# Optimization experiments

Measured on AMD Instinct MI355X. Metric: run time of the kernel, lower is better.

## Reference

```python
import jax, jax.numpy as jnp
from jax import lax
import numpy as np

RANK = 128
INPUT_DIM = 128
OUT_DIM = 32
N = 128
L = 512
INIT_STD = 1.0 / np.sqrt(RANK * INPUT_DIM)  # variance-preserving recurrence


def setup_inputs() -> dict:
    key = jax.random.key(0)
    k_x, k_A, k_a, k_O = jax.random.split(key, 4)
    x = jax.random.normal(k_x, (N, L, INPUT_DIM), dtype=jnp.float32)
    A = INIT_STD * jax.random.normal(k_A, (RANK, INPUT_DIM, RANK), dtype=jnp.float32)
    alpha = INIT_STD * jax.random.normal(k_a, (RANK,), dtype=jnp.float32)
    Omega = INIT_STD * jax.random.normal(k_O, (RANK, OUT_DIM), dtype=jnp.float32)
    return {"x": x, "alpha": alpha, "A": A, "Omega": Omega}


def reference(x, alpha, A, Omega):
    # x: [N, L, D]; alpha: [R]; A: [R, D, R]; Omega: [R, M]
    # h_0 = einsum('i,ijk,nj->nk', alpha, A, x[:,0])
    h0 = jnp.einsum('i,ijk,nj->nk', alpha, A, x[:, 0, :])

    def step(h, xt):
        # h: [N, R], xt: [N, D] -> new h: [N, R]
        h = jnp.einsum('ni,ijk,nj->nk', h, A, xt)
        return h, None

    xs = jnp.swapaxes(x, 0, 1)[1:]  # [L-1, N, D]
    h, _ = lax.scan(step, h0, xs)
    out = jnp.einsum('ni,im->nm', h, Omega)  # [N, M]
    return jnp.squeeze(out)
```

## Files before the change

kernel.cpp:

```cpp
#include <hip/hip_runtime.h>

typedef _Float16 f16;
typedef _Float16 half8 __attribute__((ext_vector_type(8)));
typedef _Float16 half4v __attribute__((ext_vector_type(4)));
typedef float f32x4 __attribute__((ext_vector_type(4)));


__global__ void k_cvt_x(const float* __restrict__ in, f16* __restrict__ out) {
    int idx = blockIdx.x * blockDim.x + threadIdx.x;
    float4 v = ((const float4*)in)[idx];
    half4v o;
    o[0] = (f16)v.x; o[1] = (f16)v.y; o[2] = (f16)v.z; o[3] = (f16)v.w;
    ((half4v*)out)[idx] = o;
}

__global__ void k_cvt_A(const float* __restrict__ A, f16* __restrict__ Af2) {
    int o = blockIdx.x * blockDim.x + threadIdx.x;
    int i = o >> 14;
    int k = (o >> 7) & 127;
    int j = o & 127;
    Af2[o] = (f16)A[(i << 14) + (j << 7) + k];
}

__device__ __forceinline__
void gemm_body(f16* lA, f16* lX, const f16* __restrict__ Af2, const f16* __restrict__ Xh,
               f16* __restrict__ B, int t0, int logTc, int qtile, int i, int tid) {
    const int row = tid >> 4;
    const int ch = tid & 15;
    const int Tcm1 = (1 << logTc) - 1;

    {
        const f16* srcA = Af2 + ((size_t)i << 14);
#pragma unroll
        for (int r = 0; r < 128; r += 16) {
            int rr = row + r;
            uint4 v = *(const uint4*)(srcA + (rr << 7) + (ch << 3));
            *(uint4*)(&lA[(rr << 7) + ((ch ^ (rr & 15)) << 3)]) = v;
        }
#pragma unroll
        for (int r = 0; r < 128; r += 16) {
            int rr = row + r;
            int qr = (qtile << 7) + rr;
            int n = qr >> logTc;
            int trel = qr & Tcm1;
            const f16* srcX = Xh + (((size_t)(n << 9) + t0 + trel) << 7);
            uint4 v = *(const uint4*)(srcX + (ch << 3));
            *(uint4*)(&lX[(rr << 7) + ((ch ^ (rr & 15)) << 3)]) = v;
        }
    }
    __syncthreads();

    const int wave = tid >> 6;
    const int lane = tid & 63;
    const int l15 = lane & 15;
    const int l4 = lane >> 4;
    f32x4 acc[8][2] = {};

#pragma unroll
    for (int ks = 0; ks < 4; ++ks) {
        const int c = (ks << 2) + l4;
        half8 afr[8], bfr[2];
#pragma unroll
        for (int mt = 0; mt < 8; ++mt) {
            int rowA = (mt << 4) + l15;
            afr[mt] = *(const half8*)(&lA[(rowA << 7) + ((c ^ l15) << 3)]);
        }
#pragma unroll
        for (int qt = 0; qt < 2; ++qt) {
            int rowX = (wave << 5) + (qt << 4) + l15;
            bfr[qt] = *(const half8*)(&lX[(rowX << 7) + ((c ^ l15) << 3)]);
        }
#pragma unroll
        for (int mt = 0; mt < 8; ++mt)
#pragma unroll
            for (int qt = 0; qt < 2; ++qt)
                acc[mt][qt] = __builtin_amdgcn_mfma_f32_16x16x32_f16(
                    afr[mt], bfr[qt], acc[mt][qt], 0, 0, 0);
    }

    __syncthreads();
    f16* stage = lA;
#pragma unroll
    for (int mt = 0; mt < 8; ++mt)
#pragma unroll
        for (int qt = 0; qt < 2; ++qt) {
            int q = (wave << 5) + (qt << 4) + l15;
            int chunk = (mt << 1) + (l4 >> 1);
            int hf = l4 & 1;
            half4v o;
            o[0] = (f16)acc[mt][qt][0];
            o[1] = (f16)acc[mt][qt][1];
            o[2] = (f16)acc[mt][qt][2];
            o[3] = (f16)acc[mt][qt][3];
            *(half4v*)(&stage[(q << 7) + (((chunk ^ l15) << 3) + (hf << 2))]) = o;
        }
    __syncthreads();
    {
        const int lr = lane >> 4;
        const int lc = lane & 15;
#pragma unroll
        for (int it = 0; it < 8; ++it) {
            int q = (wave << 5) + (it << 2) + lr;
            uint4 v = *(const uint4*)(&stage[(q << 7) + ((lc ^ (q & 15)) << 3)]);
            size_t qg = (size_t)((qtile << 7) + q);
            *(uint4*)(B + (qg << 14) + (i << 7) + (lc << 3)) = v;
        }
    }
}

__device__ __forceinline__
void chain_body(float* hl, float (*part)[132], const f16* __restrict__ B,
                float* __restrict__ hstate, const float* __restrict__ alpha,
                const float* __restrict__ Om, float* __restrict__ out,
                int Tc, int first, int last, int n, int tid) {
    const int kg = tid & 15;
    const int iq = tid >> 4;

    if (tid < 128) hl[tid] = first ? alpha[tid] : hstate[(n << 7) + tid];
    __syncthreads();

    const f16* bbase = B + (((size_t)n * Tc) << 14) + (iq << 10) + (kg << 3);
    half8 buf[4][8];
#pragma unroll
    for (int s = 0; s < 4; ++s)
#pragma unroll
        for (int ii = 0; ii < 8; ++ii)
            buf[s][ii] = *(const half8*)(bbase + ((size_t)s << 14) + (ii << 7));

    for (int t = 0; t < Tc; t += 4) {
#pragma unroll
        for (int s = 0; s < 4; ++s) {
            float4 h0 = *(const float4*)&hl[iq << 3];
            float4 h1 = *(const float4*)&hl[(iq << 3) + 4];
            float acc[8] = {0, 0, 0, 0, 0, 0, 0, 0};
#pragma unroll
            for (int ii = 0; ii < 4; ++ii) {
                float hv = (&h0.x)[ii];
#pragma unroll
                for (int j = 0; j < 8; ++j)
                    acc[j] += hv * (float)buf[s][ii][j];
            }
#pragma unroll
            for (int ii = 0; ii < 4; ++ii) {
                float hv = (&h1.x)[ii];
#pragma unroll
                for (int j = 0; j < 8; ++j)
                    acc[j] += hv * (float)buf[s][ii + 4][j];
            }
            int tn = t + s + 4;
            if (tn < Tc) {
#pragma unroll
                for (int ii = 0; ii < 8; ++ii)
                    buf[s][ii] = *(const half8*)(bbase + ((size_t)tn << 14) + (ii << 7));
            }
            *(float4*)(&part[iq][kg << 3])       = make_float4(acc[0], acc[1], acc[2], acc[3]);
            *(float4*)(&part[iq][(kg << 3) + 4]) = make_float4(acc[4], acc[5], acc[6], acc[7]);
            __syncthreads();
            if (tid < 128) {
                float s0 = part[0][tid] + part[1][tid];
                float s1 = part[2][tid] + part[3][tid];
                float s2 = part[4][tid] + part[5][tid];
                float s3 = part[6][tid] + part[7][tid];
                s0 += part[8][tid] + part[9][tid];
                s1 += part[10][tid] + part[11][tid];
                s2 += part[12][tid] + part[13][tid];
                s3 += part[14][tid] + part[15][tid];
                hl[tid] = (s0 + s1) + (s2 + s3);
            }
            __syncthreads();
        }
    }

    if (!last) {
        if (tid < 128) hstate[(n << 7) + tid] = hl[tid];
    } else if (tid < 32) {
        float s = 0.f;
        for (int i2 = 0; i2 < 128; ++i2) s += hl[i2] * Om[(i2 << 5) + tid];
        out[(n << 5) + tid] = s;
    }
}

__global__ __launch_bounds__(256, 2)
void k_gemm(const f16* __restrict__ Af2, const f16* __restrict__ Xh,
            f16* __restrict__ B, int t0, int logTc) {
    __shared__ __align__(16) char smem[65536];
    gemm_body((f16*)smem, (f16*)(smem + 32768), Af2, Xh, B, t0, logTc,
              blockIdx.x, blockIdx.y, threadIdx.x);
}

__global__ __launch_bounds__(256, 2)
void k_chain(const f16* __restrict__ B, float* __restrict__ hstate,
             const float* __restrict__ alpha, const float* __restrict__ Om,
             float* __restrict__ out, int Tc, int first, int last) {
    __shared__ __align__(16) char smem[16384];
    chain_body((float*)smem, (float(*)[132])(smem + 512), B, hstate, alpha, Om, out,
               Tc, first, last, blockIdx.x, threadIdx.x);
}

__global__ __launch_bounds__(256, 2)
void k_fused(const f16* __restrict__ Af2, const f16* __restrict__ Xh,
             f16* __restrict__ Bw, const f16* __restrict__ Br,
             float* __restrict__ hstate, const float* __restrict__ alpha,
             const float* __restrict__ Om, float* __restrict__ out,
             int t0g, int logTc, int Tc, int first, int last) {
    __shared__ __align__(16) char smem[65536];
    const int bx = blockIdx.x;
    if (bx < 128) {
        chain_body((float*)smem, (float(*)[132])(smem + 512), Br, hstate, alpha, Om, out,
                   Tc, first, last, bx, threadIdx.x);
    } else {
        int g = bx - 128;
        int qtile = g & (Tc - 1);
        int i = g >> logTc;
        gemm_body((f16*)smem, (f16*)(smem + 32768), Af2, Xh, Bw, t0g, logTc,
                  qtile, i, threadIdx.x);
    }
}

extern "C" void kernel_launch(void* const* d_in, const int* in_sizes, int n_in,
                              void* d_out, int out_size, void* d_ws, size_t ws_size,
                              hipStream_t stream) {
    const float* x     = (const float*)d_in[0];
    const float* alpha = (const float*)d_in[1];
    const float* A     = (const float*)d_in[2];
    const float* Om    = (const float*)d_in[3];
    float* out = (float*)d_out;

    char* ws = (char*)d_ws;
    f16*   Af2    = (f16*)ws;
    f16*   Xh     = (f16*)(ws + ((size_t)4 << 20));
    float* hstate = (float*)(ws + ((size_t)20 << 20));

    int Tc = 16;
    while (Tc > 4 && ((size_t)21 << 20) + (((size_t)Tc << 22) * 2) > ws_size) Tc >>= 1;
    int logTc = 31 - __builtin_clz(Tc);
    int nch = 512 / Tc;
    f16* Bc[2];
    Bc[0] = (f16*)(ws + ((size_t)21 << 20));
    Bc[1] = (f16*)(ws + ((size_t)21 << 20) + ((size_t)Tc << 22));

    k_cvt_x<<<8192, 256, 0, stream>>>(x, Xh);
    k_cvt_A<<<8192, 256, 0, stream>>>(A, Af2);

    k_gemm<<<dim3(Tc, 128), 256, 0, stream>>>(Af2, Xh, Bc[0], 0, logTc);

    for (int c = 0; c < nch; ++c) {
        const f16* br = Bc[c & 1];
        if (c + 1 < nch) {
            k_fused<<<128 + Tc * 128, 256, 0, stream>>>(
                Af2, Xh, Bc[(c + 1) & 1], br, hstate, alpha, Om, out,
                (c + 1) * Tc, logTc, Tc, c == 0, c == nch - 1);
        } else {
            k_chain<<<128, 256, 0, stream>>>(br, hstate, alpha, Om, out,
                                             Tc, c == 0, c == nch - 1);
        }
    }
    (void)in_sizes; (void)n_in; (void)out_size;
}
```

Baseline: 966.4 us.

## Double block size to 512 threads, halving per-thread work in GEMM and chain

Raises all main kernels from 256 to 512 threads per block. Each GEMM wave now computes a 16-column tile instead of 32, and each chain thread handles 4 input rows instead of 8. The chain reduction now sums 32 partial rows in shared memory instead of 16. The aim is more latency hiding and parallelism in the serial chain step, at the cost of wider barriers, a larger reduction, and possibly fewer resident blocks for the shared-memory-heavy GEMM.

```diff
diff --git a/kernel.cpp b/kernel.cpp
--- a/kernel.cpp
+++ b/kernel.cpp
@@ -32,13 +32,13 @@
     {
         const f16* srcA = Af2 + ((size_t)i << 14);
 #pragma unroll
-        for (int r = 0; r < 128; r += 16) {
+        for (int r = 0; r < 128; r += 32) {
             int rr = row + r;
             uint4 v = *(const uint4*)(srcA + (rr << 7) + (ch << 3));
             *(uint4*)(&lA[(rr << 7) + ((ch ^ (rr & 15)) << 3)]) = v;
         }
 #pragma unroll
-        for (int r = 0; r < 128; r += 16) {
+        for (int r = 0; r < 128; r += 32) {
             int rr = row + r;
             int qr = (qtile << 7) + rr;
             int n = qr >> logTc;
@@ -54,53 +54,47 @@
     const int lane = tid & 63;
     const int l15 = lane & 15;
     const int l4 = lane >> 4;
-    f32x4 acc[8][2] = {};
+    f32x4 acc[8] = {};
 
 #pragma unroll
     for (int ks = 0; ks < 4; ++ks) {
         const int c = (ks << 2) + l4;
-        half8 afr[8], bfr[2];
+        half8 afr[8], bfr;
 #pragma unroll
         for (int mt = 0; mt < 8; ++mt) {
             int rowA = (mt << 4) + l15;
             afr[mt] = *(const half8*)(&lA[(rowA << 7) + ((c ^ l15) << 3)]);
         }
-#pragma unroll
-        for (int qt = 0; qt < 2; ++qt) {
-            int rowX = (wave << 5) + (qt << 4) + l15;
-            bfr[qt] = *(const half8*)(&lX[(rowX << 7) + ((c ^ l15) << 3)]);
+        {
+            int rowX = (wave << 4) + l15;
+            bfr = *(const half8*)(&lX[(rowX << 7) + ((c ^ l15) << 3)]);
         }
 #pragma unroll
         for (int mt = 0; mt < 8; ++mt)
-#pragma unroll
-            for (int qt = 0; qt < 2; ++qt)
-                acc[mt][qt] = __builtin_amdgcn_mfma_f32_16x16x32_f16(
-                    afr[mt], bfr[qt], acc[mt][qt], 0, 0, 0);
+            acc[mt] = __builtin_amdgcn_mfma_f32_16x16x32_f16(afr[mt], bfr, acc[mt], 0, 0, 0);
     }
 
     __syncthreads();
     f16* stage = lA;
 #pragma unroll
-    for (int mt = 0; mt < 8; ++mt)
-#pragma unroll
-        for (int qt = 0; qt < 2; ++qt) {
-            int q = (wave << 5) + (qt << 4) + l15;
-            int chunk = (mt << 1) + (l4 >> 1);
-            int hf = l4 & 1;
-            half4v o;
-            o[0] = (f16)acc[mt][qt][0];
-            o[1] = (f16)acc[mt][qt][1];
-            o[2] = (f16)acc[mt][qt][2];
-            o[3] = (f16)acc[mt][qt][3];
-            *(half4v*)(&stage[(q << 7) + (((chunk ^ l15) << 3) + (hf << 2))]) = o;
-        }
+    for (int mt = 0; mt < 8; ++mt) {
+        int q = (wave << 4) + l15;
+        int chunk = (mt << 1) + (l4 >> 1);
+        int hf = l4 & 1;
+        half4v o;
+        o[0] = (f16)acc[mt][0];
+        o[1] = (f16)acc[mt][1];
+        o[2] = (f16)acc[mt][2];
+        o[3] = (f16)acc[mt][3];
+        *(half4v*)(&stage[(q << 7) + (((chunk ^ l15) << 3) + (hf << 2))]) = o;
+    }
     __syncthreads();
     {
         const int lr = lane >> 4;
         const int lc = lane & 15;
 #pragma unroll
-        for (int it = 0; it < 8; ++it) {
-            int q = (wave << 5) + (it << 2) + lr;
+        for (int it = 0; it < 4; ++it) {
+            int q = (wave << 4) + (it << 2) + lr;
             uint4 v = *(const uint4*)(&stage[(q << 7) + ((lc ^ (q & 15)) << 3)]);
             size_t qg = (size_t)((qtile << 7) + q);
             *(uint4*)(B + (qg << 14) + (i << 7) + (lc << 3)) = v;
@@ -114,24 +108,23 @@
                 const float* __restrict__ Om, float* __restrict__ out,
                 int Tc, int first, int last, int n, int tid) {
     const int kg = tid & 15;
-    const int iq = tid >> 4;
+    const int ig = tid >> 4;
 
     if (tid < 128) hl[tid] = first ? alpha[tid] : hstate[(n << 7) + tid];
     __syncthreads();
 
-    const f16* bbase = B + (((size_t)n * Tc) << 14) + (iq << 10) + (kg << 3);
-    half8 buf[4][8];
+    const f16* bbase = B + (((size_t)n * Tc) << 14) + (ig << 9) + (kg << 3);
+    half8 buf[4][4];
 #pragma unroll
     for (int s = 0; s < 4; ++s)
 #pragma unroll
-        for (int ii = 0; ii < 8; ++ii)
+        for (int ii = 0; ii < 4; ++ii)
             buf[s][ii] = *(const half8*)(bbase + ((size_t)s << 14) + (ii << 7));
 
     for (int t = 0; t < Tc; t += 4) {
 #pragma unroll
         for (int s = 0; s < 4; ++s) {
-            float4 h0 = *(const float4*)&hl[iq << 3];
-            float4 h1 = *(const float4*)&hl[(iq << 3) + 4];
+            float4 h0 = *(const float4*)&hl[ig << 2];
             float acc[8] = {0, 0, 0, 0, 0, 0, 0, 0};
 #pragma unroll
             for (int ii = 0; ii < 4; ++ii) {
@@ -140,31 +133,24 @@
                 for (int j = 0; j < 8; ++j)
                     acc[j] += hv * (float)buf[s][ii][j];
             }
-#pragma unroll
-            for (int ii = 0; ii < 4; ++ii) {
-                float hv = (&h1.x)[ii];
-#pragma unroll
-                for (int j = 0; j < 8; ++j)
-                    acc[j] += hv * (float)buf[s][ii + 4][j];
-            }
             int tn = t + s + 4;
             if (tn < Tc) {
 #pragma unroll
-                for (int ii = 0; ii < 8; ++ii)
+                for (int ii = 0; ii < 4; ++ii)
                     buf[s][ii] = *(const half8*)(bbase + ((size_t)tn << 14) + (ii << 7));
             }
-            *(float4*)(&part[iq][kg << 3])       = make_float4(acc[0], acc[1], acc[2], acc[3]);
-            *(float4*)(&part[iq][(kg << 3) + 4]) = make_float4(acc[4], acc[5], acc[6], acc[7]);
+            *(float4*)(&part[ig][kg << 3])       = make_float4(acc[0], acc[1], acc[2], acc[3]);
+            *(float4*)(&part[ig][(kg << 3) + 4]) = make_float4(acc[4], acc[5], acc[6], acc[7]);
             __syncthreads();
             if (tid < 128) {
-                float s0 = part[0][tid] + part[1][tid];
-                float s1 = part[2][tid] + part[3][tid];
-                float s2 = part[4][tid] + part[5][tid];
-                float s3 = part[6][tid] + part[7][tid];
-                s0 += part[8][tid] + part[9][tid];
-                s1 += part[10][tid] + part[11][tid];
-                s2 += part[12][tid] + part[13][tid];
-                s3 += part[14][tid] + part[15][tid];
+                float s0 = 0.f, s1 = 0.f, s2 = 0.f, s3 = 0.f;
+#pragma unroll
+                for (int p = 0; p < 32; p += 4) {
+                    s0 += part[p][tid];
+                    s1 += part[p + 1][tid];
+                    s2 += part[p + 2][tid];
+                    s3 += part[p + 3][tid];
+                }
                 hl[tid] = (s0 + s1) + (s2 + s3);
             }
             __syncthreads();
@@ -180,7 +166,7 @@
     }
 }
 
-__global__ __launch_bounds__(256, 2)
+__global__ __launch_bounds__(512, 4)
 void k_gemm(const f16* __restrict__ Af2, const f16* __restrict__ Xh,
             f16* __restrict__ B, int t0, int logTc) {
     __shared__ __align__(16) char smem[65536];
@@ -188,16 +174,16 @@
               blockIdx.x, blockIdx.y, threadIdx.x);
 }
 
-__global__ __launch_bounds__(256, 2)
+__global__ __launch_bounds__(512, 4)
 void k_chain(const f16* __restrict__ B, float* __restrict__ hstate,
              const float* __restrict__ alpha, const float* __restrict__ Om,
              float* __restrict__ out, int Tc, int first, int last) {
-    __shared__ __align__(16) char smem[16384];
+    __shared__ __align__(16) char smem[17920];
     chain_body((float*)smem, (float(*)[132])(smem + 512), B, hstate, alpha, Om, out,
                Tc, first, last, blockIdx.x, threadIdx.x);
 }
 
-__global__ __launch_bounds__(256, 2)
+__global__ __launch_bounds__(512, 4)
 void k_fused(const f16* __restrict__ Af2, const f16* __restrict__ Xh,
              f16* __restrict__ Bw, const f16* __restrict__ Br,
              float* __restrict__ hstate, const float* __restrict__ alpha,
@@ -242,16 +228,16 @@
     k_cvt_x<<<8192, 256, 0, stream>>>(x, Xh);
     k_cvt_A<<<8192, 256, 0, stream>>>(A, Af2);
 
-    k_gemm<<<dim3(Tc, 128), 256, 0, stream>>>(Af2, Xh, Bc[0], 0, logTc);
+    k_gemm<<<dim3(Tc, 128), 512, 0, stream>>>(Af2, Xh, Bc[0], 0, logTc);
 
     for (int c = 0; c < nch; ++c) {
         const f16* br = Bc[c & 1];
         if (c + 1 < nch) {
-            k_fused<<<128 + Tc * 128, 256, 0, stream>>>(
+            k_fused<<<128 + Tc * 128, 512, 0, stream>>>(
                 Af2, Xh, Bc[(c + 1) & 1], br, hstate, alpha, Om, out,
                 (c + 1) * Tc, logTc, Tc, c == 0, c == nch - 1);
         } else {
-            k_chain<<<128, 256, 0, stream>>>(br, hstate, alpha, Om, out,
+            k_chain<<<128, 512, 0, stream>>>(br, hstate, alpha, Om, out,
                                              Tc, c == 0, c == nch - 1);
         }
     }
```

Result: slower. 1.002 ms (+3.6%).

## Run each recurrence chain on a single wavefront with shuffle reduction

Applied to the files above, without the earlier changes.

The sequential h-recurrence is restructured so that each sequence is handled by one 64-lane wavefront, with four sequences per block, instead of a full 256-thread block per sequence. The partial-sum reduction now uses cross-lane shuffles and wave-local LDS writes in place of a 16-way LDS reduction guarded by two __syncthreads per step. As a result the chain occupies 32 blocks instead of 128, which frees CUs for the overlapped GEMM blocks. In exchange, the 4-step register prefetch of B is removed, so each step waits on its own global loads, and each lane now does four times more FMAs per step on the serial critical path.

```diff
diff --git a/kernel.cpp b/kernel.cpp
--- a/kernel.cpp
+++ b/kernel.cpp
@@ -109,74 +109,61 @@
 }
 
 __device__ __forceinline__
-void chain_body(float* hl, float (*part)[132], const f16* __restrict__ B,
+void chain_wave(float* hB, const f16* __restrict__ B,
                 float* __restrict__ hstate, const float* __restrict__ alpha,
                 const float* __restrict__ Om, float* __restrict__ out,
-                int Tc, int first, int last, int n, int tid) {
-    const int kg = tid & 15;
-    const int iq = tid >> 4;
-
-    if (tid < 128) hl[tid] = first ? alpha[tid] : hstate[(n << 7) + tid];
-    __syncthreads();
-
-    const f16* bbase = B + (((size_t)n * Tc) << 14) + (iq << 10) + (kg << 3);
-    half8 buf[4][8];
-#pragma unroll
-    for (int s = 0; s < 4; ++s)
-#pragma unroll
-        for (int ii = 0; ii < 8; ++ii)
-            buf[s][ii] = *(const half8*)(bbase + ((size_t)s << 14) + (ii << 7));
-
-    for (int t = 0; t < Tc; t += 4) {
-#pragma unroll
-        for (int s = 0; s < 4; ++s) {
-            float4 h0 = *(const float4*)&hl[iq << 3];
-            float4 h1 = *(const float4*)&hl[(iq << 3) + 4];
-            float acc[8] = {0, 0, 0, 0, 0, 0, 0, 0};
-#pragma unroll
-            for (int ii = 0; ii < 4; ++ii) {
-                float hv = (&h0.x)[ii];
-#pragma unroll
-                for (int j = 0; j < 8; ++j)
-                    acc[j] += hv * (float)buf[s][ii][j];
-            }
-#pragma unroll
-            for (int ii = 0; ii < 4; ++ii) {
-                float hv = (&h1.x)[ii];
-#pragma unroll
-                for (int j = 0; j < 8; ++j)
-                    acc[j] += hv * (float)buf[s][ii + 4][j];
-            }
-            int tn = t + s + 4;
-            if (tn < Tc) {
-#pragma unroll
-                for (int ii = 0; ii < 8; ++ii)
-                    buf[s][ii] = *(const half8*)(bbase + ((size_t)tn << 14) + (ii << 7));
-            }
-            *(float4*)(&part[iq][kg << 3])       = make_float4(acc[0], acc[1], acc[2], acc[3]);
-            *(float4*)(&part[iq][(kg << 3) + 4]) = make_float4(acc[4], acc[5], acc[6], acc[7]);
-            __syncthreads();
-            if (tid < 128) {
-                float s0 = part[0][tid] + part[1][tid];
-                float s1 = part[2][tid] + part[3][tid];
-                float s2 = part[4][tid] + part[5][tid];
-                float s3 = part[6][tid] + part[7][tid];
-                s0 += part[8][tid] + part[9][tid];
-                s1 += part[10][tid] + part[11][tid];
-                s2 += part[12][tid] + part[13][tid];
-                s3 += part[14][tid] + part[15][tid];
-                hl[tid] = (s0 + s1) + (s2 + s3);
-            }
-            __syncthreads();
+                int Tc, int first, int last, int n, int lane) {
+    const int iq = lane >> 4;
+    const int kg = lane & 15;
+
+    if (first) {
+        hB[lane] = alpha[lane];
+        hB[lane + 64] = alpha[lane + 64];
+    } else {
+        const float* hs = hstate + (n << 7);
+        hB[lane] = hs[lane];
+        hB[lane + 64] = hs[lane + 64];
+    }
+
+    const f16* bbat = B + (((size_t)n * Tc) << 14) + (iq << 12) + (kg << 3);
+
+    for (int t = 0; t < Tc; ++t) {
+        const f16* bt = bbat + ((size_t)t << 14);
+        float4 hv[8];
+#pragma unroll
+        for (int m = 0; m < 8; ++m)
+            hv[m] = *(const float4*)&hB[(iq << 5) + (m << 2)];
+
+        float acc[8] = {0, 0, 0, 0, 0, 0, 0, 0};
+#pragma unroll
+        for (int m = 0; m < 32; ++m) {
+            half8 b = *(const half8*)(bt + (m << 7));
+            float s = (&hv[m >> 2].x)[m & 3];
+#pragma unroll
+            for (int j = 0; j < 8; ++j)
+                acc[j] += s * (float)b[j];
+        }
+#pragma unroll
+        for (int j = 0; j < 8; ++j) {
+            float v = acc[j];
+            v += __shfl_xor(v, 16);
+            v += __shfl_xor(v, 32);
+            acc[j] = v;
+        }
+        if (iq == 0) {
+            *(float4*)&hB[(kg << 3)]     = make_float4(acc[0], acc[1], acc[2], acc[3]);
+            *(float4*)&hB[(kg << 3) + 4] = make_float4(acc[4], acc[5], acc[6], acc[7]);
         }
     }
 
     if (!last) {
-        if (tid < 128) hstate[(n << 7) + tid] = hl[tid];
-    } else if (tid < 32) {
+        float* hs = hstate + (n << 7);
+        hs[lane] = hB[lane];
+        hs[lane + 64] = hB[lane + 64];
+    } else if (lane < 32) {
         float s = 0.f;
-        for (int i2 = 0; i2 < 128; ++i2) s += hl[i2] * Om[(i2 << 5) + tid];
-        out[(n << 5) + tid] = s;
+        for (int i2 = 0; i2 < 128; ++i2) s += hB[i2] * Om[(i2 << 5) + lane];
+        out[(n << 5) + lane] = s;
     }
 }
 
@@ -192,9 +179,10 @@
 void k_chain(const f16* __restrict__ B, float* __restrict__ hstate,
              const float* __restrict__ alpha, const float* __restrict__ Om,
              float* __restrict__ out, int Tc, int first, int last) {
-    __shared__ __align__(16) char smem[16384];
-    chain_body((float*)smem, (float(*)[132])(smem + 512), B, hstate, alpha, Om, out,
-               Tc, first, last, blockIdx.x, threadIdx.x);
+    __shared__ __align__(16) float hB[4][128];
+    const int w = threadIdx.x >> 6;
+    chain_wave(hB[w], B, hstate, alpha, Om, out, Tc, first, last,
+               (blockIdx.x << 2) + w, threadIdx.x & 63);
 }
 
 __global__ __launch_bounds__(256, 2)
@@ -205,11 +193,12 @@
              int t0g, int logTc, int Tc, int first, int last) {
     __shared__ __align__(16) char smem[65536];
     const int bx = blockIdx.x;
-    if (bx < 128) {
-        chain_body((float*)smem, (float(*)[132])(smem + 512), Br, hstate, alpha, Om, out,
-                   Tc, first, last, bx, threadIdx.x);
+    if (bx < 32) {
+        float* hB = (float*)(smem + ((threadIdx.x >> 6) << 9));
+        chain_wave(hB, Br, hstate, alpha, Om, out, Tc, first, last,
+                   (bx << 2) + (threadIdx.x >> 6), threadIdx.x & 63);
     } else {
-        int g = bx - 128;
+        int g = bx - 32;
         int qtile = g & (Tc - 1);
         int i = g >> logTc;
         gemm_body((f16*)smem, (f16*)(smem + 32768), Af2, Xh, Bw, t0g, logTc,
@@ -247,12 +236,12 @@
     for (int c = 0; c < nch; ++c) {
         const f16* br = Bc[c & 1];
         if (c + 1 < nch) {
-            k_fused<<<128 + Tc * 128, 256, 0, stream>>>(
+            k_fused<<<32 + Tc * 128, 256, 0, stream>>>(
                 Af2, Xh, Bc[(c + 1) & 1], br, hstate, alpha, Om, out,
                 (c + 1) * Tc, logTc, Tc, c == 0, c == nch - 1);
         } else {
-            k_chain<<<128, 256, 0, stream>>>(br, hstate, alpha, Om, out,
-                                             Tc, c == 0, c == nch - 1);
+            k_chain<<<32, 256, 0, stream>>>(br, hstate, alpha, Om, out,
+                                            Tc, c == 0, c == nch - 1);
         }
     }
     (void)in_sizes; (void)n_in; (void)out_size;
```

Result: slower. 1.281 ms (+32.5%).
